# Kernel tuning notes

Hardware: AMD Instinct MI355X
Metric: run time of the kernel (lower is better)

Reference implementation:

```python
import jax, jax.numpy as jnp
import numpy as np

G = 8          # tileGridSize=(8,8)
CLIP = 5.0     # clipLimit
NBINS = 256


def setup_inputs() -> dict:
    key = jax.random.key(0)
    inputs = jax.random.randint(key, (128, 512, 512, 3), 0, 256).astype(jnp.float32)
    return {"inputs": inputs}


def _clahe_gray(gray):
    # gray: int32 [B,H,W] in [0,255]
    B, H, W = gray.shape
    tH, tW = H // G, W // G
    area = tH * tW
    clip_lim = max(int(CLIP * area / NBINS), 1)  # OpenCV: clipLimit*tileArea/histSize

    # per-tile 256-bin histograms via one big scatter-add
    tiles = gray.reshape(B, G, tH, G, tW).transpose(0, 1, 3, 2, 4).reshape(B * G * G, area)
    offs = jnp.arange(B * G * G, dtype=jnp.int32)[:, None] * NBINS + tiles
    hist = (jnp.zeros((B * G * G * NBINS,), jnp.float32)
            .at[offs.ravel()].add(1.0)
            .reshape(B, G, G, NBINS))

    # clip histogram, redistribute excess uniformly over all bins
    excess = jnp.sum(jnp.maximum(hist - clip_lim, 0.0), axis=-1, keepdims=True)
    histc = jnp.minimum(hist, clip_lim) + excess / NBINS

    # per-tile LUT from CDF (OpenCV: lut = round(cumsum * 255/area))
    cdf = jnp.cumsum(histc, axis=-1)
    lut = jnp.clip(jnp.round(cdf * (255.0 / area)), 0.0, 255.0)  # [B,G,G,256]

    # bilinear interpolation between 4 neighbouring tile LUTs (OpenCV: txf = x/tW - 0.5)
    xf = jnp.arange(W, dtype=jnp.float32) / tW - 0.5
    x1 = jnp.floor(xf)
    xa = xf - x1
    x1i = jnp.clip(x1.astype(jnp.int32), 0, G - 1)
    x2i = jnp.clip(x1.astype(jnp.int32) + 1, 0, G - 1)
    yf = jnp.arange(H, dtype=jnp.float32) / tH - 0.5
    y1 = jnp.floor(yf)
    ya = yf - y1
    y1i = jnp.clip(y1.astype(jnp.int32), 0, G - 1)
    y2i = jnp.clip(y1.astype(jnp.int32) + 1, 0, G - 1)

    b = jnp.arange(B)[:, None, None]
    Y1, Y2 = y1i[None, :, None], y2i[None, :, None]
    X1, X2 = x1i[None, None, :], x2i[None, None, :]
    v = gray  # pixel value indexes the LUT
    r11 = lut[b, Y1, X1, v]
    r12 = lut[b, Y1, X2, v]
    r21 = lut[b, Y2, X1, v]
    r22 = lut[b, Y2, X2, v]
    XA = xa[None, None, :]
    YA = ya[None, :, None]
    res = (r11 * (1.0 - XA) + r12 * XA) * (1.0 - YA) + (r21 * (1.0 - XA) + r22 * XA) * YA
    return jnp.clip(jnp.round(res), 0.0, 255.0)


def reference(inputs):
    # astype('uint8') of a [0,255] float image
    img = jnp.clip(inputs, 0.0, 255.0).astype(jnp.int32)
    bch, gch, rch = img[..., 0], img[..., 1], img[..., 2]  # BGR channel order
    gray = jnp.clip(jnp.round(0.114 * bch + 0.587 * gch + 0.299 * rch), 0.0, 255.0).astype(jnp.int32)
    out = _clahe_gray(gray)
    # GRAY2RGB: replicate equalized channel, return float32
    return jnp.repeat(out[..., None], 3, axis=-1).astype(jnp.float32)
```

## Files before the change

kernel.cpp:

```cpp
#include <hip/hip_runtime.h>
#include <stdint.h>

#define NB   128
#define HH   512
#define WW   512
#define IMG  (HH*WW)
#define NPIX (NB*IMG)
#define NBINS 256
#define CLIPLIM 80
#define LUT_SCALE (255.0f/4096.0f)

__device__ __forceinline__ int gray_of(float bc, float gc, float rc) {
    bc = fminf(fmaxf(bc, 0.0f), 255.0f);
    gc = fminf(fmaxf(gc, 0.0f), 255.0f);
    rc = fminf(fmaxf(rc, 0.0f), 255.0f);
    double bi = (double)(int)bc;
    double gi = (double)(int)gc;
    double ri = (double)(int)rc;
    double s = 0.114 * bi + 0.587 * gi + 0.299 * ri;
    int v = (int)rint(s);
    v = v < 0 ? 0 : (v > 255 ? 255 : v);
    return v;
}

template <bool WRITE_GRAY>
__global__ __launch_bounds__(256) void k_hist_lut(const float* __restrict__ in,
                                                  uint8_t* __restrict__ gray,
                                                  uint8_t* __restrict__ lut) {
    __shared__ int   hist[NBINS];
    __shared__ float sc[NBINS];
    __shared__ int   excess_s;
    const int t   = threadIdx.x;
    const int blk = blockIdx.x;
    const int b   = blk >> 6;
    const int ty  = (blk >> 3) & 7;
    const int tx  = blk & 7;
    const int y0  = ty * 64, x0 = tx * 64;

    hist[t] = 0;
    if (t == 0) excess_s = 0;
    __syncthreads();

    const int rwi = t >> 4;
    const int c   = (t & 15) * 4;
    #pragma unroll
    for (int it = 0; it < 4; ++it) {
        const int y = y0 + it * 16 + rwi;
        const size_t pbase = ((size_t)b * IMG + (size_t)y * WW + (x0 + c));
        const float4* p = (const float4*)(in + pbase * 3);
        float4 a0 = p[0], a1 = p[1], a2 = p[2];
        int v0 = gray_of(a0.x, a0.y, a0.z);
        int v1 = gray_of(a0.w, a1.x, a1.y);
        int v2 = gray_of(a1.z, a1.w, a2.x);
        int v3 = gray_of(a2.y, a2.z, a2.w);
        atomicAdd(&hist[v0], 1);
        atomicAdd(&hist[v1], 1);
        atomicAdd(&hist[v2], 1);
        atomicAdd(&hist[v3], 1);
        if (WRITE_GRAY)
            *(uchar4*)(gray + pbase) = make_uchar4((uint8_t)v0, (uint8_t)v1,
                                                   (uint8_t)v2, (uint8_t)v3);
    }
    __syncthreads();

    const int h = hist[t];
    atomicAdd(&excess_s, h > CLIPLIM ? h - CLIPLIM : 0);
    __syncthreads();
    const float e  = (float)excess_s * (1.0f / 256.0f);
    const float hc = (float)(h < CLIPLIM ? h : CLIPLIM) + e;

    sc[t] = hc;
    __syncthreads();
    #pragma unroll
    for (int off = 1; off < NBINS; off <<= 1) {
        float add = (t >= off) ? sc[t - off] : 0.0f;
        __syncthreads();
        sc[t] += add;
        __syncthreads();
    }
    float l = rintf(__fmul_rn(sc[t], LUT_SCALE));
    l = fminf(fmaxf(l, 0.0f), 255.0f);
    lut[blk * NBINS + t] = (uint8_t)l;
}

__device__ __forceinline__ float4 bilerp_group(const uint8_t* __restrict__ lut,
                                               int b, int y, int x,
                                               const int vv[4]) {
    const int   y1  = (y - 32) >> 6;
    const float ya  = (float)((y + 32) & 63) * (1.0f/64.0f);
    const int   y1i = y1 < 0 ? 0 : y1;
    const int   y2i = (y1 + 1) > 7 ? 7 : (y1 + 1);
    const uint8_t* lb  = lut + b * (64 * NBINS);
    const uint8_t* lr1 = lb + y1i * (8 * NBINS);
    const uint8_t* lr2 = lb + y2i * (8 * NBINS);
    const float iya = __fsub_rn(1.0f, ya);

    float res[4];
    #pragma unroll
    for (int j = 0; j < 4; ++j) {
        const int xx  = x + j;
        const int x1  = (xx - 32) >> 6;
        const float xa  = (float)((xx + 32) & 63) * (1.0f/64.0f);
        const int  x1i = x1 < 0 ? 0 : x1;
        const int  x2i = (x1 + 1) > 7 ? 7 : (x1 + 1);
        const int  v   = vv[j];
        const float r11 = (float)lr1[x1i * NBINS + v];
        const float r12 = (float)lr1[x2i * NBINS + v];
        const float r21 = (float)lr2[x1i * NBINS + v];
        const float r22 = (float)lr2[x2i * NBINS + v];
        const float ixa = __fsub_rn(1.0f, xa);
        const float top = __fadd_rn(__fmul_rn(r11, ixa), __fmul_rn(r12, xa));
        const float bot = __fadd_rn(__fmul_rn(r21, ixa), __fmul_rn(r22, xa));
        float r = __fadd_rn(__fmul_rn(top, iya), __fmul_rn(bot, ya));
        r = rintf(r);
        res[j] = fminf(fmaxf(r, 0.0f), 255.0f);
    }
    return make_float4(res[0], res[1], res[2], res[3]);
}

__device__ __forceinline__ void store_group(float* __restrict__ out, int pix, float4 r) {
    float4* o = (float4*)(out + (size_t)pix * 3);
    o[0] = make_float4(r.x, r.x, r.x, r.y);
    o[1] = make_float4(r.y, r.y, r.z, r.z);
    o[2] = make_float4(r.z, r.w, r.w, r.w);
}

__global__ __launch_bounds__(256) void k_apply(const uint8_t* __restrict__ gray,
                                               const uint8_t* __restrict__ lut,
                                               float* __restrict__ out) {
    const int nG = NPIX / 4;
    for (int g = blockIdx.x * blockDim.x + threadIdx.x; g < nG;
         g += gridDim.x * blockDim.x) {
        const int pix = g << 2;
        const int b   = pix >> 18;
        const int rem = pix & (IMG - 1);
        const int y   = rem >> 9;
        const int x   = rem & (WW - 1);
        const uchar4 v4 = ((const uchar4*)gray)[g];
        const int vv[4] = {v4.x, v4.y, v4.z, v4.w};
        store_group(out, pix, bilerp_group(lut, b, y, x, vv));
    }
}

__global__ __launch_bounds__(256) void k_apply_recompute(const float* __restrict__ in,
                                                         const uint8_t* __restrict__ lut,
                                                         float* __restrict__ out) {
    const int nG = NPIX / 4;
    for (int g = blockIdx.x * blockDim.x + threadIdx.x; g < nG;
         g += gridDim.x * blockDim.x) {
        const int pix = g << 2;
        const int b   = pix >> 18;
        const int rem = pix & (IMG - 1);
        const int y   = rem >> 9;
        const int x   = rem & (WW - 1);
        const float4* p = (const float4*)(in + (size_t)pix * 3);
        float4 a0 = p[0], a1 = p[1], a2 = p[2];
        const int vv[4] = {gray_of(a0.x, a0.y, a0.z), gray_of(a0.w, a1.x, a1.y),
                           gray_of(a1.z, a1.w, a2.x), gray_of(a2.y, a2.z, a2.w)};
        store_group(out, pix, bilerp_group(lut, b, y, x, vv));
    }
}

extern "C" void kernel_launch(void* const* d_in, const int* in_sizes, int n_in,
                              void* d_out, int out_size, void* d_ws, size_t ws_size,
                              hipStream_t stream) {
    const float* in  = (const float*)d_in[0];
    float*       out = (float*)d_out;
    const size_t lut_bytes  = (size_t)NB * 64 * NBINS;
    const size_t gray_bytes = (size_t)NPIX;

    if (ws_size >= gray_bytes + lut_bytes) {
        uint8_t* gray = (uint8_t*)d_ws;
        uint8_t* lut  = (uint8_t*)d_ws + gray_bytes;
        k_hist_lut<true><<<NB * 64, 256, 0, stream>>>(in, gray, lut);
        k_apply<<<8192, 256, 0, stream>>>(gray, lut, out);
    } else {
        uint8_t* lut = (uint8_t*)d_ws;
        k_hist_lut<false><<<NB * 64, 256, 0, stream>>>(in, nullptr, lut);
        k_apply_recompute<<<8192, 256, 0, stream>>>(in, lut, out);
    }
}
```

Measured before the change: 775.8 us.

## Stage per-row tile LUTs in shared memory and coalesce output stores via LDS

Replaces the grid-stride apply kernel with one block per two image rows. Each block copies the 8-tile LUT rows it needs into shared memory, so the four gathers per pixel read LDS instead of global memory. Outputs are staged in a padded shared buffer and written as fully coalesced float4 stores. This adds two barriers and extra shared-memory traffic per block, which may limit occupancy.

```diff
diff --git a/kernel.cpp b/kernel.cpp
--- a/kernel.cpp
+++ b/kernel.cpp
@@ -83,6 +83,84 @@
     lut[blk * NBINS + t] = (uint8_t)l;
 }
 
+__global__ __launch_bounds__(256) void k_apply2(const uint8_t* __restrict__ gray,
+                                                const uint8_t* __restrict__ lut,
+                                                float* __restrict__ out) {
+    __shared__ uint8_t lut_s[4][2048];
+    __shared__ float   outs[256 * 13];
+
+    const int t   = threadIdx.x;
+    const int idx = blockIdx.x;
+    const int b   = idx >> 8;
+    const int y0  = (idx & 255) << 1;
+
+    float ya_r[2];
+    const uint8_t* src[4];
+    #pragma unroll
+    for (int r = 0; r < 2; ++r) {
+        const int y   = y0 + r;
+        const int y1  = (y - 32) >> 6;
+        const int y1i = y1 < 0 ? 0 : y1;
+        const int y2i = (y1 + 1) > 7 ? 7 : (y1 + 1);
+        ya_r[r] = (float)((y + 32) & 63) * (1.0f / 64.0f);
+        src[2*r]   = lut + ((b << 6) + (y1i << 3)) * 256;
+        src[2*r+1] = lut + ((b << 6) + (y2i << 3)) * 256;
+    }
+
+    {
+        const int r   = t >> 6;
+        const int off = (t & 63) * 32;
+        const uint4* s = (const uint4*)(src[r] + off);
+        uint4 a = s[0], c2 = s[1];
+        *(uint4*)(&lut_s[r][off])      = a;
+        *(uint4*)(&lut_s[r][off + 16]) = c2;
+    }
+    __syncthreads();
+
+    const int h  = t >> 7;
+    const int xb = (t & 127) << 2;
+    const float ya  = ya_r[h];
+    const float iya = __fsub_rn(1.0f, ya);
+    const uint8_t* l1 = lut_s[2*h];
+    const uint8_t* l2 = lut_s[2*h + 1];
+
+    const uchar4 v4 = ((const uchar4*)gray)[idx * 256 + t];
+    const int vv[4] = {v4.x, v4.y, v4.z, v4.w};
+
+    #pragma unroll
+    for (int j = 0; j < 4; ++j) {
+        const int xx  = xb + j;
+        const int x1  = (xx - 32) >> 6;
+        const float xa  = (float)((xx + 32) & 63) * (1.0f/64.0f);
+        const int  x1i = x1 < 0 ? 0 : x1;
+        const int  x2i = (x1 + 1) > 7 ? 7 : (x1 + 1);
+        const int  v   = vv[j];
+        const float r11 = (float)l1[(x1i << 8) + v];
+        const float r12 = (float)l1[(x2i << 8) + v];
+        const float r21 = (float)l2[(x1i << 8) + v];
+        const float r22 = (float)l2[(x2i << 8) + v];
+        const float ixa = __fsub_rn(1.0f, xa);
+        const float top = __fadd_rn(__fmul_rn(r11, ixa), __fmul_rn(r12, xa));
+        const float bot = __fadd_rn(__fmul_rn(r21, ixa), __fmul_rn(r22, xa));
+        float r = rintf(__fadd_rn(__fmul_rn(top, iya), __fmul_rn(bot, ya)));
+        r = fminf(fmaxf(r, 0.0f), 255.0f);
+        outs[t * 13 + 3*j + 0] = r;
+        outs[t * 13 + 3*j + 1] = r;
+        outs[t * 13 + 3*j + 2] = r;
+    }
+    __syncthreads();
+
+    float4* og = (float4*)out + (size_t)idx * 768;
+    #pragma unroll
+    for (int i = 0; i < 3; ++i) {
+        const int k    = t + (i << 8);
+        const int slot = k / 3;
+        const int c    = (k - slot * 3) * 4;
+        const float* p = &outs[slot * 13 + c];
+        og[k] = make_float4(p[0], p[1], p[2], p[3]);
+    }
+}
+
 __device__ __forceinline__ float4 bilerp_group(const uint8_t* __restrict__ lut,
                                                int b, int y, int x,
                                                const int vv[4]) {
@@ -94,7 +172,6 @@
     const uint8_t* lr1 = lb + y1i * (8 * NBINS);
     const uint8_t* lr2 = lb + y2i * (8 * NBINS);
     const float iya = __fsub_rn(1.0f, ya);
-
     float res[4];
     #pragma unroll
     for (int j = 0; j < 4; ++j) {
@@ -118,30 +195,6 @@
     return make_float4(res[0], res[1], res[2], res[3]);
 }
 
-__device__ __forceinline__ void store_group(float* __restrict__ out, int pix, float4 r) {
-    float4* o = (float4*)(out + (size_t)pix * 3);
-    o[0] = make_float4(r.x, r.x, r.x, r.y);
-    o[1] = make_float4(r.y, r.y, r.z, r.z);
-    o[2] = make_float4(r.z, r.w, r.w, r.w);
-}
-
-__global__ __launch_bounds__(256) void k_apply(const uint8_t* __restrict__ gray,
-                                               const uint8_t* __restrict__ lut,
-                                               float* __restrict__ out) {
-    const int nG = NPIX / 4;
-    for (int g = blockIdx.x * blockDim.x + threadIdx.x; g < nG;
-         g += gridDim.x * blockDim.x) {
-        const int pix = g << 2;
-        const int b   = pix >> 18;
-        const int rem = pix & (IMG - 1);
-        const int y   = rem >> 9;
-        const int x   = rem & (WW - 1);
-        const uchar4 v4 = ((const uchar4*)gray)[g];
-        const int vv[4] = {v4.x, v4.y, v4.z, v4.w};
-        store_group(out, pix, bilerp_group(lut, b, y, x, vv));
-    }
-}
-
 __global__ __launch_bounds__(256) void k_apply_recompute(const float* __restrict__ in,
                                                          const uint8_t* __restrict__ lut,
                                                          float* __restrict__ out) {
@@ -157,7 +210,11 @@
         float4 a0 = p[0], a1 = p[1], a2 = p[2];
         const int vv[4] = {gray_of(a0.x, a0.y, a0.z), gray_of(a0.w, a1.x, a1.y),
                            gray_of(a1.z, a1.w, a2.x), gray_of(a2.y, a2.z, a2.w)};
-        store_group(out, pix, bilerp_group(lut, b, y, x, vv));
+        float4 r = bilerp_group(lut, b, y, x, vv);
+        float4* o = (float4*)(out + (size_t)pix * 3);
+        o[0] = make_float4(r.x, r.x, r.x, r.y);
+        o[1] = make_float4(r.y, r.y, r.z, r.z);
+        o[2] = make_float4(r.z, r.w, r.w, r.w);
     }
 }
 
@@ -173,7 +230,7 @@
         uint8_t* gray = (uint8_t*)d_ws;
         uint8_t* lut  = (uint8_t*)d_ws + gray_bytes;
         k_hist_lut<true><<<NB * 64, 256, 0, stream>>>(in, gray, lut);
-        k_apply<<<8192, 256, 0, stream>>>(gray, lut, out);
+        k_apply2<<<NPIX / 1024, 256, 0, stream>>>(gray, lut, out);
     } else {
         uint8_t* lut = (uint8_t*)d_ws;
         k_hist_lut<false><<<NB * 64, 256, 0, stream>>>(in, nullptr, lut);
```

After: 704.2 us. 9.2% less time.
